# Performance work log

Measured on AMD Instinct MI355X. Metric: run time of the kernel, lower is better.

## Reference

```python
import jax, jax.numpy as jnp
import numpy as np

N_WIRES = 8


def setup_inputs() -> dict:
    key = jax.random.key(0)
    k1, k2, k3 = jax.random.split(key, 3)
    B, S, E = 8, 1024, 64
    x = jax.random.normal(k1, (B, S, E), jnp.float32)
    theta = jax.random.normal(k2, (N_WIRES,), jnp.float32) * 0.1  # trainable RX angles (shared QLayer across heads)
    V_CAT = 16
    combine_w = jax.random.normal(k3, (E, V_CAT), jnp.float32) / jnp.sqrt(jnp.float32(V_CAT))
    combine_b = jnp.zeros((E,), jnp.float32)
    return {"x": x, "theta": theta, "combine_w": combine_w, "combine_b": combine_b}


def _cnot(state, c, t):
    # state: [N] + [2]*N_WIRES ; wire w lives on axis w+1
    ca, ta = c + 1, t + 1
    s0 = jax.lax.index_in_dim(state, 0, axis=ca, keepdims=False)
    s1 = jax.lax.index_in_dim(state, 1, axis=ca, keepdims=False)
    ta2 = ta - 1 if ta > ca else ta  # control axis was removed
    s1 = jnp.flip(s1, axis=ta2)      # flip target bit where control == 1
    return jnp.stack([s0, s1], axis=ca)


def _qlayer(angles, theta):
    # angles: [N, 8]. RX(x) then trainable RX(theta) on same wire == RX(x+theta).
    half = 0.5 * (angles + theta)
    amp0 = jnp.cos(half).astype(jnp.complex64)          # <0|RX|0>
    amp1 = (-1j) * jnp.sin(half).astype(jnp.complex64)  # <1|RX|0>
    N = angles.shape[0]
    # product state over 8 wires -> [N, 256]
    state = jnp.ones((N, 1), jnp.complex64)
    for w in range(N_WIRES):
        per = jnp.stack([amp0[:, w], amp1[:, w]], axis=-1)  # [N, 2]
        state = (state[:, :, None] * per[:, None, :]).reshape(N, -1)
    state = state.reshape((N,) + (2,) * N_WIRES)
    # CNOT chain 0->1, ..., 6->7, then ring closure 7->0
    for w in range(N_WIRES - 1):
        state = _cnot(state, w, w + 1)
    state = _cnot(state, N_WIRES - 1, 0)
    probs = state.real ** 2 + state.imag ** 2
    exps = []
    for w in range(N_WIRES):
        axes = tuple(ax for ax in range(1, N_WIRES + 1) if ax != w + 1)
        marg = probs.sum(axis=axes)  # [N, 2]
        exps.append(marg[:, 0] - marg[:, 1])  # <Z_w>
    return jnp.stack(exps, axis=-1)  # [N, 8]


def reference(x, theta, combine_w, combine_b):
    B, S, E = x.shape
    d_k = E // N_WIRES  # == 8 (encoder needs exactly 8 angles)
    heads = x.reshape(B, S, N_WIRES, d_k).transpose(0, 2, 1, 3)  # [B, H, S, 8]
    meas = _qlayer(heads.reshape(-1, d_k), theta).reshape(B, N_WIRES, S, N_WIRES)
    # torch.chunk(3, -1) on size 8 -> splits of 3, 3, 2
    q, k, v = meas[..., :3], meas[..., 3:6], meas[..., 6:]
    scores = jnp.einsum('bhsd,bhtd->bhst', q, k) / jnp.sqrt(jnp.float32(E))
    attn = jax.nn.softmax(scores, axis=-1)
    out = jnp.einsum('bhst,bhtd->bhsd', attn, v)          # [B, H, S, 2]
    out = out.transpose(0, 2, 1, 3).reshape(B, S, -1)     # [B, S, 16]
    return out @ combine_w.T + combine_b
```

## Files before the change

### kernel.cpp

```cpp
#include <hip/hip_runtime.h>
#include <hip/hip_fp16.h>

#define NB 8
#define NS 1024
#define NH 8
#define NMONO 56
#define MPART 512


constexpr int PRED[NMONO] = {
    0,
    0, 0, 0,
    1, 2, 3, 2, 3, 3,
    4, 5, 6, 7, 8, 9, 7, 8, 9, 9,
    10,11,12,13,14,15,16,17,18,19,16,17,18,19,19,
    20,21,22,23,24,25,26,27,28,29,30,31,32,33,34,30,31,32,33,34,34};
constexpr int VARI[NMONO] = {
    0,
    0, 1, 2,
    0, 0, 0, 1, 1, 2,
    0, 0, 0, 0, 0, 0, 1, 1, 1, 2,
    0, 0, 0, 0, 0, 0, 0, 0, 0, 0, 1, 1, 1, 1, 2,
    0, 0, 0, 0, 0, 0, 0, 0, 0, 0, 0, 0, 0, 0, 0, 1, 1, 1, 1, 1, 2};
#define F6 0.166666666666667f
#define F12 0.0833333333333333f
#define F24 0.0416666666666667f
#define F120 0.00833333333333333f
constexpr float COEF[NMONO] = {
    1.f,
    1.f, 1.f, 1.f,
    0.5f, 1.f, 1.f, 0.5f, 1.f, 0.5f,
    F6, 0.5f, 0.5f, 0.5f, 1.f, 0.5f, F6, 0.5f, 0.5f, F6,
    F24, F6, F6, 0.25f, 0.5f, 0.25f, F6, 0.5f, 0.5f, F6, F24, F6, 0.25f, F6, F24,
    F120, F24, F24, F12, F6, F12, F12, 0.25f, 0.25f, F12, F24, F6, 0.25f, F6, F24,
    F120, F24, F12, F12, F24, F120};

__global__ __launch_bounds__(256, 2) void moments_kernel(
        const float* __restrict__ x, const float* __restrict__ theta,
        float* __restrict__ part) {
    __shared__ float4 kv4[128];
    __shared__ float  v1l[128];
    __shared__ float  red[3][64][57];

    const int tid = threadIdx.x;
    const int bh = blockIdx.x >> 3;
    const int qt = blockIdx.x & 7;
    const int b = bh >> 3, h = bh & 7;
    const int t0 = qt * 128;

    if (tid < 128) {
        float th[8];
#pragma unroll
        for (int j = 0; j < 8; ++j) th[j] = theta[j];
        int t = t0 + tid;
        const float4* xp = (const float4*)(x + ((size_t)(b * NS + t)) * 64 + h * 8);
        float4 lo = xp[0], hi = xp[1];
        float c0 = __cosf(lo.x + th[0]);
        float c1 = __cosf(lo.y + th[1]);
        float c2 = __cosf(lo.z + th[2]);
        float c3 = __cosf(lo.w + th[3]);
        float c4 = __cosf(hi.x + th[4]);
        float c5 = __cosf(hi.y + th[5]);
        float c6 = __cosf(hi.z + th[6]);
        float c7 = __cosf(hi.w + th[7]);
        float m3 = ((c0 * c1) * c2) * c3;
        float m4 = m3 * c4;
        float m5 = m4 * c5;
        float m6 = m5 * c6;
        kv4[tid] = make_float4(m3, m4, m5, m6);
        v1l[tid] = m6 * c7;
    }
    __syncthreads();

    const int w = tid >> 6, l = tid & 63;
    if (w < 3) {
        float acc[NMONO];
#pragma unroll
        for (int i = 0; i < NMONO; ++i) acc[i] = 0.f;
#pragma unroll 1
        for (int j = 0; j < 2; ++j) {
            float4 kv = kv4[l + 64 * j];
            float v1 = v1l[l + 64 * j];
            float wch = (w == 0) ? 1.f : ((w == 1) ? kv.w : v1);
            float mono[NMONO];
            mono[0] = wch;
            acc[0] += wch;
#pragma unroll
            for (int i = 1; i < NMONO; ++i) {
                float var = (VARI[i] == 0) ? kv.x : ((VARI[i] == 1) ? kv.y : kv.z);
                mono[i] = mono[PRED[i]] * var;
                acc[i] += mono[i];
            }
        }
#pragma unroll
        for (int i = 0; i < NMONO; ++i) red[w][l][i] = acc[i];
    }
    __syncthreads();

    if (w < 3 && l < NMONO) {
        float s0 = 0.f, s1 = 0.f, s2 = 0.f, s3 = 0.f;
#pragma unroll
        for (int r = 0; r < 16; ++r) {
            s0 += red[w][4 * r + 0][l];
            s1 += red[w][4 * r + 1][l];
            s2 += red[w][4 * r + 2][l];
            s3 += red[w][4 * r + 3][l];
        }
        part[(size_t)blockIdx.x * 168 + w * 56 + l] = ((s0 + s1) + (s2 + s3)) * COEF[l];
    }
}

__global__ __launch_bounds__(256, 1) void eval_proj_kernel(
        const float* __restrict__ x, const float* __restrict__ theta,
        const float* __restrict__ part, const float* __restrict__ W,
        const float* __restrict__ bias, float* __restrict__ out) {
    __shared__ __align__(16) float MhL[8 * 172];
    __shared__ float WtL[16 * 65];
    __shared__ float biasL[64];
    __shared__ float attL[32][17];

    const int tid = threadIdx.x;
    const int b = blockIdx.x >> 5;
    const int sc = blockIdx.x & 31;
    const int s0 = sc * 32;

    for (int e = tid; e < 8 * 168; e += 256) {
        int h = e / 168, idx = e - h * 168;
        const float* p = part + ((size_t)((b * 8 + h) * 8)) * 168 + idx;
        float s = ((p[0] + p[168]) + (p[336] + p[504]))
                + ((p[672] + p[840]) + (p[1008] + p[1176]));
        MhL[h * 172 + idx] = s;
    }
    for (int i = tid; i < 1024; i += 256) WtL[(i & 15) * 65 + (i >> 4)] = W[i];
    if (tid < 64) biasL[tid] = bias[tid];
    __syncthreads();

    {
        const int h = tid >> 5, sl = tid & 31;
        const int s = s0 + sl;
        float th[8];
#pragma unroll
        for (int j = 0; j < 8; ++j) th[j] = theta[j];
        const float4* xp = (const float4*)(x + ((size_t)(b * NS + s)) * 64 + h * 8);
        float4 lo = xp[0], hi = xp[1];
        float c0 = __cosf(lo.x + th[0]);
        float c1 = __cosf(lo.y + th[1]);
        float c2 = __cosf(lo.z + th[2]);
        float c3 = __cosf(lo.w + th[3]);
        float c4 = __cosf(hi.x + th[4]);
        float c5 = __cosf(hi.y + th[5]);
        float c6 = __cosf(hi.z + th[6]);
        float c7 = __cosf(hi.w + th[7]);
        float m1 = c0 * c1;
        float m2 = m1 * c2;
        float m0 = ((c1 * c2) * (c3 * c4)) * ((c5 * c6) * c7);
        float q0 = m0 * 0.125f, q1 = m1 * 0.125f, q2 = m2 * 0.125f;

        float mono[NMONO];
        mono[0] = 1.f;
#pragma unroll
        for (int i = 1; i < NMONO; ++i)
            mono[i] = mono[PRED[i]] * ((VARI[i] == 0) ? q0 : ((VARI[i] == 1) ? q1 : q2));

        const float4* MS = (const float4*)&MhL[h * 172];
        const float4* MA = (const float4*)&MhL[h * 172 + 56];
        const float4* MB = (const float4*)&MhL[h * 172 + 112];
        float aS = 0.f, aA = 0.f, aB = 0.f;
#pragma unroll
        for (int g = 0; g < 14; ++g) {
            float4 ms = MS[g], ma = MA[g], mb = MB[g];
            float p0 = mono[g * 4 + 0], p1 = mono[g * 4 + 1];
            float p2 = mono[g * 4 + 2], p3 = mono[g * 4 + 3];
            aS = fmaf(p0, ms.x, aS); aS = fmaf(p1, ms.y, aS);
            aS = fmaf(p2, ms.z, aS); aS = fmaf(p3, ms.w, aS);
            aA = fmaf(p0, ma.x, aA); aA = fmaf(p1, ma.y, aA);
            aA = fmaf(p2, ma.z, aA); aA = fmaf(p3, ma.w, aA);
            aB = fmaf(p0, mb.x, aB); aB = fmaf(p1, mb.y, aB);
            aB = fmaf(p2, mb.z, aB); aB = fmaf(p3, mb.w, aB);
        }
        float inv = 1.0f / aS;
        attL[sl][2 * h]     = aA * inv;
        attL[sl][2 * h + 1] = aB * inv;
    }
    __syncthreads();

    {
        const int e = tid & 63, rr = tid >> 6;
#pragma unroll
        for (int j = 0; j < 8; ++j) {
            int row = rr * 8 + j;
            float acc = biasL[e];
#pragma unroll
            for (int jj = 0; jj < 16; ++jj)
                acc = fmaf(attL[row][jj], WtL[jj * 65 + e], acc);
            out[((size_t)(b * NS + s0 + row)) * 64 + e] = acc;
        }
    }
}

#define NPAD 1028
#define SPB 32
__global__ __launch_bounds__(256) void fused_kernel(const float* __restrict__ x,
                                                    const float* __restrict__ theta,
                                                    const float* __restrict__ W,
                                                    const float* __restrict__ bias,
                                                    float* __restrict__ out) {
    __shared__ __half2 kvA[NH][NPAD];
    __shared__ __half2 kvB[NH][NPAD];
    __shared__ __half  kvC[NH][NPAD];
    __shared__ float   attl[SPB][17];
    __shared__ float   Wt[16][64];
    __shared__ float   bl[64];

    const int tid = threadIdx.x;
    const int b = blockIdx.x >> 5;
    const int chunk = blockIdx.x & 31;

    float th[8];
#pragma unroll
    for (int j = 0; j < 8; ++j) th[j] = theta[j];

    for (int i = tid; i < 1024; i += 256) Wt[i & 15][i >> 4] = W[i];
    if (tid < 64) bl[tid] = bias[tid];

    for (int i = 0; i < 32; ++i) {
        int r = tid + (i << 8);
        int h = r & 7, t = r >> 3;
        const float4* xp = (const float4*)(x + (((size_t)(b * NS + t)) << 6) + h * 8);
        float4 lo = xp[0], hi = xp[1];
        float c0 = __cosf(lo.x + th[0]);
        float c1 = __cosf(lo.y + th[1]);
        float c2 = __cosf(lo.z + th[2]);
        float c3 = __cosf(lo.w + th[3]);
        float c4 = __cosf(hi.x + th[4]);
        float c5 = __cosf(hi.y + th[5]);
        float c6 = __cosf(hi.z + th[6]);
        float c7 = __cosf(hi.w + th[7]);
        float m3 = ((c0 * c1) * c2) * c3;
        float m4 = m3 * c4;
        float m5 = m4 * c5;
        float m6 = m5 * c6;
        float m7 = m6 * c7;
        kvA[h][t] = __floats2half2_rn(m3, m4);
        kvB[h][t] = __floats2half2_rn(m5, m6);
        kvC[h][t] = __float2half_rn(m7);
    }
    __syncthreads();

    {
        const int h = tid >> 5;
        const int sl = tid & 31;
        const int sg = chunk * SPB + sl;
        const float4* xp = (const float4*)(x + (((size_t)(b * NS + sg)) << 6) + h * 8);
        float4 lo = xp[0], hi = xp[1];
        float c0 = __cosf(lo.x + th[0]);
        float c1 = __cosf(lo.y + th[1]);
        float c2 = __cosf(lo.z + th[2]);
        float c3 = __cosf(lo.w + th[3]);
        float c4 = __cosf(hi.x + th[4]);
        float c5 = __cosf(hi.y + th[5]);
        float c6 = __cosf(hi.z + th[6]);
        float c7 = __cosf(hi.w + th[7]);
        float m1 = c0 * c1;
        float m2 = m1 * c2;
        float m0 = ((c1 * c2) * (c3 * c4)) * ((c5 * c6) * c7);
        float q0 = m0 * 0.125f, q1 = m1 * 0.125f, q2 = m2 * 0.125f;

        float sum = 0.f, a0 = 0.f, a1 = 0.f;
#pragma unroll 4
        for (int t = 0; t < NS; ++t) {
            float2 kk = __half22float2(kvA[h][t]);
            float2 kv = __half22float2(kvB[h][t]);
            float v1 = __half2float(kvC[h][t]);
            float sc = q0 * kk.x + q1 * kk.y + q2 * kv.x;
            float e = __expf(sc);
            sum += e;
            a0 += e * kv.y;
            a1 += e * v1;
        }
        float inv = 1.0f / sum;
        attl[sl][h * 2] = a0 * inv;
        attl[sl][h * 2 + 1] = a1 * inv;
    }
    __syncthreads();

    {
        const int e = tid & 63;
        const int rr = tid >> 6;
#pragma unroll
        for (int i = 0; i < 8; ++i) {
            int sl = rr * 8 + i;
            float acc = bl[e];
#pragma unroll
            for (int j = 0; j < 16; ++j)
                acc += attl[sl][j] * Wt[j][e];
            int sg = chunk * SPB + sl;
            out[(((size_t)(b * NS + sg)) << 6) + e] = acc;
        }
    }
}

extern "C" void kernel_launch(void* const* d_in, const int* in_sizes, int n_in,
                              void* d_out, int out_size, void* d_ws, size_t ws_size,
                              hipStream_t stream) {
    const float* x     = (const float*)d_in[0];
    const float* theta = (const float*)d_in[1];
    const float* W     = (const float*)d_in[2];
    const float* bias  = (const float*)d_in[3];
    float* out = (float*)d_out;

    if (ws_size >= (size_t)MPART * 168 * sizeof(float)) {
        float* part = (float*)d_ws;
        moments_kernel<<<dim3(MPART), dim3(256), 0, stream>>>(x, theta, part);
        eval_proj_kernel<<<dim3(256), dim3(256), 0, stream>>>(x, theta, part, W, bias, out);
    } else {
        fused_kernel<<<dim3(NB * (NS / SPB)), dim3(256), 0, stream>>>(x, theta, W, bias, out);
    }
}
```

Measured before the change: 69.91 us.

## Recompute cosines per warp in moments kernel and halve eval tile size

```diff
diff --git a/kernel.cpp b/kernel.cpp
--- a/kernel.cpp
+++ b/kernel.cpp
@@ -35,12 +35,10 @@
     F120, F24, F24, F12, F6, F12, F12, 0.25f, 0.25f, F12, F24, F6, 0.25f, F6, F24,
     F120, F24, F12, F12, F24, F120};
 
-__global__ __launch_bounds__(256, 2) void moments_kernel(
+__global__ __launch_bounds__(192) void moments_kernel(
         const float* __restrict__ x, const float* __restrict__ theta,
         float* __restrict__ part) {
-    __shared__ float4 kv4[128];
-    __shared__ float  v1l[128];
-    __shared__ float  red[3][64][57];
+    __shared__ float red[3][64][57];
 
     const int tid = threadIdx.x;
     const int bh = blockIdx.x >> 3;
@@ -48,11 +46,19 @@
     const int b = bh >> 3, h = bh & 7;
     const int t0 = qt * 128;
 
-    if (tid < 128) {
-        float th[8];
-#pragma unroll
-        for (int j = 0; j < 8; ++j) th[j] = theta[j];
-        int t = t0 + tid;
+    float th[8];
+#pragma unroll
+    for (int j = 0; j < 8; ++j) th[j] = theta[j];
+
+    const int w = tid >> 6, l = tid & 63;
+
+    float acc[NMONO];
+#pragma unroll
+    for (int i = 0; i < NMONO; ++i) acc[i] = 0.f;
+
+#pragma unroll 1
+    for (int j = 0; j < 2; ++j) {
+        int t = t0 + l + 64 * j;
         const float4* xp = (const float4*)(x + ((size_t)(b * NS + t)) * 64 + h * 8);
         float4 lo = xp[0], hi = xp[1];
         float c0 = __cosf(lo.x + th[0]);
@@ -63,41 +69,28 @@
         float c5 = __cosf(hi.y + th[5]);
         float c6 = __cosf(hi.z + th[6]);
         float c7 = __cosf(hi.w + th[7]);
-        float m3 = ((c0 * c1) * c2) * c3;
-        float m4 = m3 * c4;
-        float m5 = m4 * c5;
-        float m6 = m5 * c6;
-        kv4[tid] = make_float4(m3, m4, m5, m6);
-        v1l[tid] = m6 * c7;
-    }
-    __syncthreads();
-
-    const int w = tid >> 6, l = tid & 63;
-    if (w < 3) {
-        float acc[NMONO];
-#pragma unroll
-        for (int i = 0; i < NMONO; ++i) acc[i] = 0.f;
-#pragma unroll 1
-        for (int j = 0; j < 2; ++j) {
-            float4 kv = kv4[l + 64 * j];
-            float v1 = v1l[l + 64 * j];
-            float wch = (w == 0) ? 1.f : ((w == 1) ? kv.w : v1);
-            float mono[NMONO];
-            mono[0] = wch;
-            acc[0] += wch;
-#pragma unroll
-            for (int i = 1; i < NMONO; ++i) {
-                float var = (VARI[i] == 0) ? kv.x : ((VARI[i] == 1) ? kv.y : kv.z);
-                mono[i] = mono[PRED[i]] * var;
-                acc[i] += mono[i];
-            }
-        }
-#pragma unroll
-        for (int i = 0; i < NMONO; ++i) red[w][l][i] = acc[i];
-    }
-    __syncthreads();
-
-    if (w < 3 && l < NMONO) {
+        float k0 = ((c0 * c1) * c2) * c3;
+        float k1 = k0 * c4;
+        float k2 = k1 * c5;
+        float v0 = k2 * c6;
+        float v1 = v0 * c7;
+        float wch = (w == 0) ? 1.f : ((w == 1) ? v0 : v1);
+
+        float mono[NMONO];
+        mono[0] = wch;
+        acc[0] += wch;
+#pragma unroll
+        for (int i = 1; i < NMONO; ++i) {
+            float var = (VARI[i] == 0) ? k0 : ((VARI[i] == 1) ? k1 : k2);
+            mono[i] = mono[PRED[i]] * var;
+            acc[i] += mono[i];
+        }
+    }
+#pragma unroll
+    for (int i = 0; i < NMONO; ++i) red[w][l][i] = acc[i];
+    __syncthreads();
+
+    if (l < NMONO) {
         float s0 = 0.f, s1 = 0.f, s2 = 0.f, s3 = 0.f;
 #pragma unroll
         for (int r = 0; r < 16; ++r) {
@@ -110,19 +103,19 @@
     }
 }
 
-__global__ __launch_bounds__(256, 1) void eval_proj_kernel(
+__global__ __launch_bounds__(256) void eval_proj_kernel(
         const float* __restrict__ x, const float* __restrict__ theta,
         const float* __restrict__ part, const float* __restrict__ W,
         const float* __restrict__ bias, float* __restrict__ out) {
     __shared__ __align__(16) float MhL[8 * 172];
     __shared__ float WtL[16 * 65];
     __shared__ float biasL[64];
-    __shared__ float attL[32][17];
+    __shared__ float attL[16][17];
 
     const int tid = threadIdx.x;
-    const int b = blockIdx.x >> 5;
-    const int sc = blockIdx.x & 31;
-    const int s0 = sc * 32;
+    const int b = blockIdx.x >> 6;
+    const int sc = blockIdx.x & 63;
+    const int s0 = sc * 16;
 
     for (int e = tid; e < 8 * 168; e += 256) {
         int h = e / 168, idx = e - h * 168;
@@ -135,8 +128,8 @@
     if (tid < 64) biasL[tid] = bias[tid];
     __syncthreads();
 
-    {
-        const int h = tid >> 5, sl = tid & 31;
+    if (tid < 128) {
+        const int h = tid >> 4, sl = tid & 15;
         const int s = s0 + sl;
         float th[8];
 #pragma unroll
@@ -187,8 +180,8 @@
     {
         const int e = tid & 63, rr = tid >> 6;
 #pragma unroll
-        for (int j = 0; j < 8; ++j) {
-            int row = rr * 8 + j;
+        for (int j = 0; j < 4; ++j) {
+            int row = rr * 4 + j;
             float acc = biasL[e];
 #pragma unroll
             for (int jj = 0; jj < 16; ++jj)
@@ -311,8 +304,8 @@
 
     if (ws_size >= (size_t)MPART * 168 * sizeof(float)) {
         float* part = (float*)d_ws;
-        moments_kernel<<<dim3(MPART), dim3(256), 0, stream>>>(x, theta, part);
-        eval_proj_kernel<<<dim3(256), dim3(256), 0, stream>>>(x, theta, part, W, bias, out);
+        moments_kernel<<<dim3(MPART), dim3(192), 0, stream>>>(x, theta, part);
+        eval_proj_kernel<<<dim3(512), dim3(256), 0, stream>>>(x, theta, part, W, bias, out);
     } else {
         fused_kernel<<<dim3(NB * (NS / SPB)), dim3(256), 0, stream>>>(x, theta, W, bias, out);
     }
```

New measurement: 69.27 us (median of 2 runs). No clear change (-0.9%).
